# Kernel tuning notes

Measured on AMD Instinct MI355X. Metric: run time of the kernel, lower is better.

Reference implementation:

```python
import jax, jax.numpy as jnp
import numpy as np

H = 4096        # hidden_size
NH = 32         # num query heads
NKV = 8         # num kv heads
HD = H // NH    # head_dim = 128
T_PREV = 16383  # cached tokens; new token makes T = 16384
BASE = 10000.0


def _rope(x, pos):
    # x: [heads, head_dim]; interleaved even/odd RoPE at a single position
    d = x.shape[-1]
    inv_freq = 1.0 / (BASE ** (jnp.arange(0, d, 2, dtype=jnp.float32) / d))
    f = pos * inv_freq                      # [d/2]
    c, s = jnp.cos(f), jnp.sin(f)
    xe, xo = x[..., 0::2], x[..., 1::2]
    out = jnp.stack([xe * c - xo * s, xe * s + xo * c], axis=-1)
    return out.reshape(x.shape)


def setup_inputs() -> dict:
    key = jax.random.key(0)
    ks = jax.random.split(key, 7)
    w = 0.02  # weight scale for numerical stability
    return {
        "hidden": jax.random.normal(ks[0], (H,), jnp.float32),
        "k_cache": jax.random.normal(ks[1], (T_PREV, NKV, HD), jnp.float32),
        "v_cache": jax.random.normal(ks[2], (T_PREV, NKV, HD), jnp.float32),
        "Wq": jax.random.normal(ks[3], (H, H), jnp.float32) * w,
        "Wk": jax.random.normal(ks[4], (NKV * HD, H), jnp.float32) * w,
        "Wv": jax.random.normal(ks[5], (NKV * HD, H), jnp.float32) * w,
        "Wo": jax.random.normal(ks[6], (H, H), jnp.float32) * w,
        "position_id": T_PREV,
    }


def reference(hidden, k_cache, v_cache, Wq, Wk, Wv, Wo, position_id):
    pos = jnp.float32(position_id)
    # projections (nn.Linear: y = W @ x), single token
    q = (Wq @ hidden).reshape(NH, HD)
    k = (Wk @ hidden).reshape(NKV, HD)
    v = (Wv @ hidden).reshape(NKV, HD)
    # inline RoPE on new q and k
    q = _rope(q, pos)
    k = _rope(k, pos)
    # contiguous KV including the new token
    k_all = jnp.concatenate([k_cache, k[None]], axis=0)   # [T, NKV, HD]
    v_all = jnp.concatenate([v_cache, v[None]], axis=0)
    # GQA: repeat KV heads to match query heads
    rep = NH // NKV
    k_all = jnp.repeat(k_all, rep, axis=1)                 # [T, NH, HD]
    v_all = jnp.repeat(v_all, rep, axis=1)
    # single-query attention
    scores = jnp.einsum('hd,thd->ht', q, k_all) / jnp.sqrt(jnp.float32(HD))
    attn = jax.nn.softmax(scores, axis=-1)                 # [NH, T]
    ctx = jnp.einsum('ht,thd->hd', attn, v_all)            # [NH, HD]
    # combine heads + output projection
    return Wo @ ctx.reshape(H)
```

## Files before the change

kernel.cpp:

```cpp
#include <hip/hip_runtime.h>
#include <math.h>
#include <stdint.h>

#define NH 32
#define NKV 8
#define HD 128
#define HDIM 4096
#define KVDIM 1024
#define TPREV 16383
#define NCHUNK 256
#define CHUNK 64

#define OFF_Q 0
#define OFF_K 4096
#define OFF_V 5120
#define OFF_PART 6144
#define PART_STRIDE 132
#define OFF_CTX (OFF_PART + NH * NCHUNK * PART_STRIDE)

__device__ __forceinline__ float wave_reduce_sum(float v) {
#pragma unroll
  for (int m = 32; m >= 1; m >>= 1) v += __shfl_xor(v, m, 64);
  return v;
}
__device__ __forceinline__ float wave_reduce_max(float v) {
#pragma unroll
  for (int m = 32; m >= 1; m >>= 1) v = fmaxf(v, __shfl_xor(v, m, 64));
  return v;
}
__device__ __forceinline__ float dot4(float4 a, float4 b) {
  return a.x * b.x + a.y * b.y + a.z * b.z + a.w * b.w;
}

typedef const __attribute__((address_space(1))) unsigned int* gld_gp;
typedef __attribute__((address_space(3))) unsigned int* gld_lp;
__device__ __forceinline__ void cp16(const float* g, float* l) {
  __builtin_amdgcn_global_load_lds((gld_gp)(uintptr_t)g,
                                   (gld_lp)(uint32_t)(uintptr_t)l, 16, 0, 0);
}

__global__ __launch_bounds__(256) void qkv_rope_kernel(
    const float* __restrict__ Wq, const float* __restrict__ Wk,
    const float* __restrict__ Wv, const float* __restrict__ hidden,
    const int* __restrict__ pos_p, float* __restrict__ ws) {
  int r = blockIdx.x * 4 + (threadIdx.x >> 6);
  int lane = threadIdx.x & 63;
  const float* W;
  int wr;
  if (r < HDIM) {
    W = Wq; wr = r;
  } else if (r < HDIM + KVDIM) {
    W = Wk; wr = r - HDIM;
  } else {
    W = Wv; wr = r - HDIM - KVDIM;
  }
  const float4* w4 = (const float4*)(W + (size_t)wr * HDIM);
  const float4* h4 = (const float4*)hidden;
  float s = 0.f;
#pragma unroll
  for (int base = 0; base < 16; base += 8) {
    float4 a[8], b[8];
#pragma unroll
    for (int j = 0; j < 8; ++j) a[j] = w4[lane + 64 * (base + j)];
#pragma unroll
    for (int j = 0; j < 8; ++j) b[j] = h4[lane + 64 * (base + j)];
#pragma unroll
    for (int j = 0; j < 8; ++j) s += dot4(a[j], b[j]);
  }
  s = wave_reduce_sum(s);
  __shared__ float rs[4];
  if (lane == 0) rs[threadIdx.x >> 6] = s;
  __syncthreads();
  if (threadIdx.x < 2) {
    int r0 = blockIdx.x * 4 + (int)threadIdx.x * 2;
    float S0 = rs[threadIdx.x * 2], S1 = rs[threadIdx.x * 2 + 1];
    if (r0 < HDIM + KVDIM) {
      int j = (r0 & (HD - 1)) >> 1;
      double lowp = 1.0;
      if (j & 1) lowp *= 0.8659643233600653;
      if (j & 2) lowp *= 0.7498942093324559;
      if (j & 4) lowp *= 0.5623413251903491;
      if (j & 8) lowp *= 0.31622776601683794;
      double hi = (j & 16) ? 0.1 : 1.0;
      if (j & 32) hi *= 0.01;
      double f = (double)(*pos_p) * (lowp * hi);
      double k2 = floor(f * 0.15915494309189535);
      double rr = f - k2 * 6.283185307179586;
      float fr = (float)rr;
      float c = cosf(fr), sn = sinf(fr);
      ws[r0] = S0 * c - S1 * sn;
      ws[r0 + 1] = S0 * sn + S1 * c;
    } else {
      ws[r0] = S0;
      ws[r0 + 1] = S1;
    }
  }
}

__global__ __launch_bounds__(256, 4) void attn_chunk_kernel(
    const float* __restrict__ k_cache, const float* __restrict__ v_cache,
    float* __restrict__ ws) {
  int g = blockIdx.x >> 8;
  int c = blockIdx.x & 255;
  int t0 = c * CHUNK;
  int tid = threadIdx.x;
  int l = tid & 63, w = tid >> 6;

  __shared__ __align__(16) float Klds[CHUNK * HD];
  __shared__ __align__(16) float qs[4 * HD];
  __shared__ float sc[CHUNK * 5];
  __shared__ float wredm[4][4], wredl[4][4];

  if (w < 2)
    cp16(ws + OFF_Q + (g << 9) + (w << 8) + (l << 2), qs + (w << 8));
#pragma unroll
  for (int i = 0; i < 8; ++i) {
    int tokA = (w << 4) + 2 * i;
    int toks = tokA + (l >> 5);
    int gt = t0 + toks;
    if (gt >= TPREV) gt = 0;
    cp16(k_cache + (size_t)gt * KVDIM + g * HD + (((l & 31) ^ (toks & 7)) << 2),
         Klds + (tokA << 7));
  }
  __syncthreads();

  const float rscale = 0.08838834764831845f;
  int tokl = (w << 4) + (l & 15);
  int qq = l >> 4;
  int t7 = tokl & 7;
  const float4* K4 = (const float4*)Klds;
  const float4* q4 = (const float4*)qs;
  float s0 = 0.f, s1 = 0.f, s2 = 0.f, s3 = 0.f;
#pragma unroll
  for (int j = 0; j < 8; ++j) {
    float4 kk = K4[(tokl << 5) + (qq << 3) + (j ^ t7)];
    float4 qa = q4[0 * 32 + (qq << 3) + j];
    float4 qb = q4[1 * 32 + (qq << 3) + j];
    float4 qc = q4[2 * 32 + (qq << 3) + j];
    float4 qd_ = q4[3 * 32 + (qq << 3) + j];
    s0 += dot4(kk, qa); s1 += dot4(kk, qb);
    s2 += dot4(kk, qc); s3 += dot4(kk, qd_);
  }
  s0 += __shfl_xor(s0, 16, 64); s0 += __shfl_xor(s0, 32, 64);
  s1 += __shfl_xor(s1, 16, 64); s1 += __shfl_xor(s1, 32, 64);
  s2 += __shfl_xor(s2, 16, 64); s2 += __shfl_xor(s2, 32, 64);
  s3 += __shfl_xor(s3, 16, 64); s3 += __shfl_xor(s3, 32, 64);
  s0 *= rscale; s1 *= rscale; s2 *= rscale; s3 *= rscale;
  if (t0 + tokl >= TPREV) {
    s0 = -1e30f; s1 = -1e30f; s2 = -1e30f; s3 = -1e30f;
  }

  float m0 = wave_reduce_max(s0), m1 = wave_reduce_max(s1);
  float m2 = wave_reduce_max(s2), m3 = wave_reduce_max(s3);
  if (l == 0) {
    wredm[w][0] = m0; wredm[w][1] = m1; wredm[w][2] = m2; wredm[w][3] = m3;
  }
  __syncthreads();
  float mh0 = fmaxf(fmaxf(wredm[0][0], wredm[1][0]),
                    fmaxf(wredm[2][0], wredm[3][0]));
  float mh1 = fmaxf(fmaxf(wredm[0][1], wredm[1][1]),
                    fmaxf(wredm[2][1], wredm[3][1]));
  float mh2 = fmaxf(fmaxf(wredm[0][2], wredm[1][2]),
                    fmaxf(wredm[2][2], wredm[3][2]));
  float mh3 = fmaxf(fmaxf(wredm[0][3], wredm[1][3]),
                    fmaxf(wredm[2][3], wredm[3][3]));

  float e0 = expf(s0 - mh0), e1 = expf(s1 - mh1);
  float e2 = expf(s2 - mh2), e3 = expf(s3 - mh3);
  if (qq == 0) {
    sc[tokl * 5 + 0] = e0; sc[tokl * 5 + 1] = e1;
    sc[tokl * 5 + 2] = e2; sc[tokl * 5 + 3] = e3;
  }
  float l0 = 0.25f * wave_reduce_sum(e0), l1 = 0.25f * wave_reduce_sum(e1);
  float l2 = 0.25f * wave_reduce_sum(e2), l3 = 0.25f * wave_reduce_sum(e3);
  if (l == 0) {
    wredl[w][0] = l0; wredl[w][1] = l1; wredl[w][2] = l2; wredl[w][3] = l3;
  }
  __syncthreads();

  int grp = tid >> 5, d4 = tid & 31;
  float4 acc0 = {0, 0, 0, 0}, acc1 = {0, 0, 0, 0};
  float4 acc2 = {0, 0, 0, 0}, acc3 = {0, 0, 0, 0};
  const float4 z4 = {0, 0, 0, 0};
#pragma unroll
  for (int base = 0; base < 8; base += 4) {
    float4 vv[4];
#pragma unroll
    for (int j = 0; j < 4; ++j) {
      int it = grp + 8 * (base + j);
      int t = t0 + it;
      vv[j] = (t < TPREV)
                  ? ((const float4*)(v_cache + (size_t)t * KVDIM + g * HD))[d4]
                  : z4;
    }
#pragma unroll
    for (int j = 0; j < 4; ++j) {
      int it = grp + 8 * (base + j);
      float p0 = sc[it * 5 + 0], p1 = sc[it * 5 + 1];
      float p2 = sc[it * 5 + 2], p3 = sc[it * 5 + 3];
      acc0.x = fmaf(p0, vv[j].x, acc0.x); acc0.y = fmaf(p0, vv[j].y, acc0.y);
      acc0.z = fmaf(p0, vv[j].z, acc0.z); acc0.w = fmaf(p0, vv[j].w, acc0.w);
      acc1.x = fmaf(p1, vv[j].x, acc1.x); acc1.y = fmaf(p1, vv[j].y, acc1.y);
      acc1.z = fmaf(p1, vv[j].z, acc1.z); acc1.w = fmaf(p1, vv[j].w, acc1.w);
      acc2.x = fmaf(p2, vv[j].x, acc2.x); acc2.y = fmaf(p2, vv[j].y, acc2.y);
      acc2.z = fmaf(p2, vv[j].z, acc2.z); acc2.w = fmaf(p2, vv[j].w, acc2.w);
      acc3.x = fmaf(p3, vv[j].x, acc3.x); acc3.y = fmaf(p3, vv[j].y, acc3.y);
      acc3.z = fmaf(p3, vv[j].z, acc3.z); acc3.w = fmaf(p3, vv[j].w, acc3.w);
    }
  }
  float4* vacc4 = (float4*)Klds;
  vacc4[(grp * 4 + 0) * 32 + d4] = acc0;
  vacc4[(grp * 4 + 1) * 32 + d4] = acc1;
  vacc4[(grp * 4 + 2) * 32 + d4] = acc2;
  vacc4[(grp * 4 + 3) * 32 + d4] = acc3;
  __syncthreads();

  if (tid < 128) {
    int h = tid >> 5, dd = tid & 31;
    float4 s = {0, 0, 0, 0};
#pragma unroll
    for (int g2 = 0; g2 < 8; ++g2) {
      float4 v = vacc4[(g2 * 4 + h) * 32 + dd];
      s.x += v.x; s.y += v.y; s.z += v.z; s.w += v.w;
    }
    float* dst = ws + OFF_PART +
                 ((size_t)(g * 4 + h) * NCHUNK + c) * PART_STRIDE + (dd << 2);
    *(float4*)dst = s;
  }
  if (tid < 4) {
    float mh = fmaxf(fmaxf(wredm[0][tid], wredm[1][tid]),
                     fmaxf(wredm[2][tid], wredm[3][tid]));
    float lh = wredl[0][tid] + wredl[1][tid] + wredl[2][tid] + wredl[3][tid];
    float* base =
        ws + OFF_PART + ((size_t)(g * 4 + tid) * NCHUNK + c) * PART_STRIDE;
    base[128] = mh;
    base[129] = lh;
  }
}

__global__ __launch_bounds__(256) void combine_kernel(float* __restrict__ ws) {
  int h = blockIdx.x;
  int g = h >> 2;
  int tid = threadIdx.x;
  const float rscale = 0.08838834764831845f;
  const float* ph = ws + OFF_PART + (size_t)h * NCHUNK * PART_STRIDE;

  __shared__ float red[HD];
  __shared__ float wexp[NCHUNK];
  __shared__ float wm[4], wl[4];
  __shared__ float acc2[HD];

  if (tid < HD) red[tid] = ws[OFF_Q + h * HD + tid] * ws[OFF_K + g * HD + tid];
  __syncthreads();
#pragma unroll
  for (int s2 = 64; s2 >= 1; s2 >>= 1) {
    if (tid < s2 && tid + s2 < HD) red[tid] += red[tid + s2];
    __syncthreads();
  }
  float snew = red[0] * rscale;

  float mv = ph[(size_t)tid * PART_STRIDE + 128];
  float lv = ph[(size_t)tid * PART_STRIDE + 129];
  float mw = wave_reduce_max(mv);
  if ((tid & 63) == 0) wm[tid >> 6] = mw;
  __syncthreads();
  float M = fmaxf(fmaxf(fmaxf(wm[0], wm[1]), fmaxf(wm[2], wm[3])), snew);
  float w = expf(mv - M);
  wexp[tid] = w;
  float lw = wave_reduce_sum(lv * w);
  if ((tid & 63) == 0) wl[tid >> 6] = lw;
  __syncthreads();
  float en = expf(snew - M);
  float L = wl[0] + wl[1] + wl[2] + wl[3] + en;

  int half = tid >> 7, d = tid & 127;
  float acc = 0.f;
  int cbeg = half * (NCHUNK / 2);
#pragma unroll 8
  for (int c2 = cbeg; c2 < cbeg + NCHUNK / 2; ++c2)
    acc = fmaf(ph[(size_t)c2 * PART_STRIDE + d], wexp[c2], acc);
  if (half == 0) acc2[d] = acc;
  __syncthreads();
  if (half == 1) acc2[d] += acc;
  __syncthreads();
  if (tid < HD)
    ws[OFF_CTX + h * HD + tid] =
        (acc2[tid] + en * ws[OFF_V + g * HD + tid]) / L;
}

__global__ __launch_bounds__(256) void out_matvec_kernel(
    const float* __restrict__ Wo, const float* __restrict__ ws,
    float* __restrict__ out) {
  int r = blockIdx.x * 4 + (threadIdx.x >> 6);
  int lane = threadIdx.x & 63;
  const float4* w4 = (const float4*)(Wo + (size_t)r * HDIM);
  const float4* x4 = (const float4*)(ws + OFF_CTX);
  float s = 0.f;
#pragma unroll
  for (int base = 0; base < 16; base += 8) {
    float4 a[8], b[8];
#pragma unroll
    for (int j = 0; j < 8; ++j) a[j] = w4[lane + 64 * (base + j)];
#pragma unroll
    for (int j = 0; j < 8; ++j) b[j] = x4[lane + 64 * (base + j)];
#pragma unroll
    for (int j = 0; j < 8; ++j) s += dot4(a[j], b[j]);
  }
  s = wave_reduce_sum(s);
  if (lane == 0) out[r] = s;
}

extern "C" void kernel_launch(void* const* d_in, const int* in_sizes, int n_in,
                              void* d_out, int out_size, void* d_ws,
                              size_t ws_size, hipStream_t stream) {
  const float* hidden = (const float*)d_in[0];
  const float* k_cache = (const float*)d_in[1];
  const float* v_cache = (const float*)d_in[2];
  const float* Wq = (const float*)d_in[3];
  const float* Wk = (const float*)d_in[4];
  const float* Wv = (const float*)d_in[5];
  const float* Wo = (const float*)d_in[6];
  const int* pos = (const int*)d_in[7];
  float* out = (float*)d_out;
  float* ws = (float*)d_ws;

  qkv_rope_kernel<<<(HDIM + 2 * KVDIM) / 4, 256, 0, stream>>>(Wq, Wk, Wv,
                                                              hidden, pos, ws);
  attn_chunk_kernel<<<NKV * NCHUNK, 256, 0, stream>>>(k_cache, v_cache, ws);
  combine_kernel<<<NH, 256, 0, stream>>>(ws);
  out_matvec_kernel<<<HDIM / 4, 256, 0, stream>>>(Wo, ws, out);
}
```

Measured before the change: 292.5 us.

## Split attention chunk kernel into separate QK and PV kernels

```diff
diff --git a/kernel.cpp b/kernel.cpp
--- a/kernel.cpp
+++ b/kernel.cpp
@@ -17,6 +17,7 @@
 #define OFF_PART 6144
 #define PART_STRIDE 132
 #define OFF_CTX (OFF_PART + NH * NCHUNK * PART_STRIDE)
+#define OFF_SC (OFF_CTX + HDIM)
 
 __device__ __forceinline__ float wave_reduce_sum(float v) {
 #pragma unroll
@@ -97,9 +98,8 @@
   }
 }
 
-__global__ __launch_bounds__(256, 4) void attn_chunk_kernel(
-    const float* __restrict__ k_cache, const float* __restrict__ v_cache,
-    float* __restrict__ ws) {
+__global__ __launch_bounds__(256, 4) void attn_qk_kernel(
+    const float* __restrict__ k_cache, float* __restrict__ ws) {
   int g = blockIdx.x >> 8;
   int c = blockIdx.x & 255;
   int t0 = c * CHUNK;
@@ -108,7 +108,7 @@
 
   __shared__ __align__(16) float Klds[CHUNK * HD];
   __shared__ __align__(16) float qs[4 * HD];
-  __shared__ float sc[CHUNK * 5];
+  __shared__ float scl[CHUNK * 5];
   __shared__ float wredm[4][4], wredl[4][4];
 
   if (w < 2)
@@ -168,8 +168,8 @@
   float e0 = expf(s0 - mh0), e1 = expf(s1 - mh1);
   float e2 = expf(s2 - mh2), e3 = expf(s3 - mh3);
   if (qq == 0) {
-    sc[tokl * 5 + 0] = e0; sc[tokl * 5 + 1] = e1;
-    sc[tokl * 5 + 2] = e2; sc[tokl * 5 + 3] = e3;
+    scl[tokl * 5 + 0] = e0; scl[tokl * 5 + 1] = e1;
+    scl[tokl * 5 + 2] = e2; scl[tokl * 5 + 3] = e3;
   }
   float l0 = 0.25f * wave_reduce_sum(e0), l1 = 0.25f * wave_reduce_sum(e1);
   float l2 = 0.25f * wave_reduce_sum(e2), l3 = 0.25f * wave_reduce_sum(e3);
@@ -178,26 +178,54 @@
   }
   __syncthreads();
 
+  {
+    int h = tid >> 6, tok = tid & 63;
+    ws[OFF_SC + ((((size_t)g * NCHUNK + c) * 4 + h) << 6) + tok] =
+        scl[tok * 5 + h];
+  }
+  if (tid < 4) {
+    float mh = fmaxf(fmaxf(wredm[0][tid], wredm[1][tid]),
+                     fmaxf(wredm[2][tid], wredm[3][tid]));
+    float lh = wredl[0][tid] + wredl[1][tid] + wredl[2][tid] + wredl[3][tid];
+    float* base =
+        ws + OFF_PART + ((size_t)(g * 4 + tid) * NCHUNK + c) * PART_STRIDE;
+    base[128] = mh;
+    base[129] = lh;
+  }
+}
+
+__global__ __launch_bounds__(256, 4) void attn_pv_kernel(
+    const float* __restrict__ v_cache, float* __restrict__ ws) {
+  int g = blockIdx.x >> 8;
+  int c = blockIdx.x & 255;
+  int t0 = c * CHUNK;
+  int tid = threadIdx.x;
+
+  __shared__ float sc2[4 * 64];
+  __shared__ __align__(16) float vacc[8 * 4 * HD];
+
+  sc2[tid] = ws[OFF_SC + (((size_t)g * NCHUNK + c) << 8) + tid];
+  __syncthreads();
+
   int grp = tid >> 5, d4 = tid & 31;
   float4 acc0 = {0, 0, 0, 0}, acc1 = {0, 0, 0, 0};
   float4 acc2 = {0, 0, 0, 0}, acc3 = {0, 0, 0, 0};
   const float4 z4 = {0, 0, 0, 0};
-#pragma unroll
-  for (int base = 0; base < 8; base += 4) {
-    float4 vv[4];
-#pragma unroll
-    for (int j = 0; j < 4; ++j) {
-      int it = grp + 8 * (base + j);
+  {
+    float4 vv[8];
+#pragma unroll
+    for (int j = 0; j < 8; ++j) {
+      int it = grp + 8 * j;
       int t = t0 + it;
       vv[j] = (t < TPREV)
                   ? ((const float4*)(v_cache + (size_t)t * KVDIM + g * HD))[d4]
                   : z4;
     }
 #pragma unroll
-    for (int j = 0; j < 4; ++j) {
-      int it = grp + 8 * (base + j);
-      float p0 = sc[it * 5 + 0], p1 = sc[it * 5 + 1];
-      float p2 = sc[it * 5 + 2], p3 = sc[it * 5 + 3];
+    for (int j = 0; j < 8; ++j) {
+      int it = grp + 8 * j;
+      float p0 = sc2[0 * 64 + it], p1 = sc2[1 * 64 + it];
+      float p2 = sc2[2 * 64 + it], p3 = sc2[3 * 64 + it];
       acc0.x = fmaf(p0, vv[j].x, acc0.x); acc0.y = fmaf(p0, vv[j].y, acc0.y);
       acc0.z = fmaf(p0, vv[j].z, acc0.z); acc0.w = fmaf(p0, vv[j].w, acc0.w);
       acc1.x = fmaf(p1, vv[j].x, acc1.x); acc1.y = fmaf(p1, vv[j].y, acc1.y);
@@ -208,7 +236,7 @@
       acc3.z = fmaf(p3, vv[j].z, acc3.z); acc3.w = fmaf(p3, vv[j].w, acc3.w);
     }
   }
-  float4* vacc4 = (float4*)Klds;
+  float4* vacc4 = (float4*)vacc;
   vacc4[(grp * 4 + 0) * 32 + d4] = acc0;
   vacc4[(grp * 4 + 1) * 32 + d4] = acc1;
   vacc4[(grp * 4 + 2) * 32 + d4] = acc2;
@@ -227,15 +255,6 @@
                  ((size_t)(g * 4 + h) * NCHUNK + c) * PART_STRIDE + (dd << 2);
     *(float4*)dst = s;
   }
-  if (tid < 4) {
-    float mh = fmaxf(fmaxf(wredm[0][tid], wredm[1][tid]),
-                     fmaxf(wredm[2][tid], wredm[3][tid]));
-    float lh = wredl[0][tid] + wredl[1][tid] + wredl[2][tid] + wredl[3][tid];
-    float* base =
-        ws + OFF_PART + ((size_t)(g * 4 + tid) * NCHUNK + c) * PART_STRIDE;
-    base[128] = mh;
-    base[129] = lh;
-  }
 }
 
 __global__ __launch_bounds__(256) void combine_kernel(float* __restrict__ ws) {
@@ -276,9 +295,14 @@
   int half = tid >> 7, d = tid & 127;
   float acc = 0.f;
   int cbeg = half * (NCHUNK / 2);
-#pragma unroll 8
-  for (int c2 = cbeg; c2 < cbeg + NCHUNK / 2; ++c2)
-    acc = fmaf(ph[(size_t)c2 * PART_STRIDE + d], wexp[c2], acc);
+  for (int cb = cbeg; cb < cbeg + NCHUNK / 2; cb += 8) {
+    float vp[8];
+#pragma unroll
+    for (int j = 0; j < 8; ++j)
+      vp[j] = ph[(size_t)(cb + j) * PART_STRIDE + d];
+#pragma unroll
+    for (int j = 0; j < 8; ++j) acc = fmaf(vp[j], wexp[cb + j], acc);
+  }
   if (half == 0) acc2[d] = acc;
   __syncthreads();
   if (half == 1) acc2[d] += acc;
@@ -326,7 +350,8 @@
 
   qkv_rope_kernel<<<(HDIM + 2 * KVDIM) / 4, 256, 0, stream>>>(Wq, Wk, Wv,
                                                               hidden, pos, ws);
-  attn_chunk_kernel<<<NKV * NCHUNK, 256, 0, stream>>>(k_cache, v_cache, ws);
+  attn_qk_kernel<<<NKV * NCHUNK, 256, 0, stream>>>(k_cache, ws);
+  attn_pv_kernel<<<NKV * NCHUNK, 256, 0, stream>>>(v_cache, ws);
   combine_kernel<<<NH, 256, 0, stream>>>(ws);
   out_matvec_kernel<<<HDIM / 4, 256, 0, stream>>>(Wo, ws, out);
 }
```

New measurement: 296.1 us. About the same (+1.2%).
